# Kernel tuning notes

Hardware: AMD Instinct MI355X
Metric: run time of the kernel (lower is better)

## Reference

```python
import jax, jax.numpy as jnp
import numpy as np

NQ, DEPTH = 4, 2
C64 = jnp.complex64


def _ry(theta):
    # theta: scalar or (B,) -> (...,2,2) complex
    h = theta.astype(jnp.float32) / 2
    c, s = jnp.cos(h).astype(C64), jnp.sin(h).astype(C64)
    return jnp.stack([jnp.stack([c, -s], -1), jnp.stack([s, c], -1)], -2)


def _rot(phi, theta, omega):
    # PennyLane Rot = RZ(omega) @ RY(theta) @ RZ(phi), scalars -> (2,2) complex
    h = theta / 2
    c, s = jnp.cos(h), jnp.sin(h)
    ep = jnp.exp(-0.5j * (phi + omega).astype(C64))
    em = jnp.exp(0.5j * (phi - omega).astype(C64))
    return jnp.array(1.0, C64) * jnp.stack([
        jnp.stack([ep * c, -em * s], -1),
        jnp.stack([jnp.conj(em) * s, jnp.conj(ep) * c], -1)], -2)


def _apply_1q(state, U, wire):
    # state: (B,2,2,2,2); U: (2,2) or (B,2,2)
    s = jnp.moveaxis(state, wire + 1, -1)
    if U.ndim == 2:
        s = jnp.einsum('ij,bklmj->bklmi', U, s)
    else:
        s = jnp.einsum('bij,bklmj->bklmi', U, s)
    return jnp.moveaxis(s, -1, wire + 1)


def _cnot(state, ctrl, tgt):
    s = jnp.moveaxis(state, [ctrl + 1, tgt + 1], [-2, -1])
    s = s.at[..., 1, :].set(s[..., 1, ::-1])
    return jnp.moveaxis(s, [-2, -1], [ctrl + 1, tgt + 1])


def _circuit(x, q_weights):
    B = x.shape[0]
    state = jnp.zeros((B, 2, 2, 2, 2), C64).at[:, 0, 0, 0, 0].set(1.0)
    # angle encoding: RY(x[:, w]) on wire w (batched gates)
    for w in range(NQ):
        state = _apply_1q(state, _ry(x[:, w]), w)
    # variational layers
    for layer in range(DEPTH):
        for w in range(NQ):
            U = _rot(q_weights[layer, w, 0], q_weights[layer, w, 1], q_weights[layer, w, 2])
            state = _apply_1q(state, U, w)
        for w in range(NQ - 1):
            state = _cnot(state, w, w + 1)
        state = _cnot(state, NQ - 1, 0)  # num_qubits > 2 wrap-around
    # expval PauliZ on each wire
    probs = jnp.abs(state) ** 2  # (B,2,2,2,2) float32
    z = jnp.array([1.0, -1.0], jnp.float32)
    outs = [jnp.einsum('bijkl,' + 'ijkl'[w] + '->b', probs, z) for w in range(NQ)]
    return jnp.stack(outs, axis=1).astype(x.dtype)  # (B, 4)


def setup_inputs() -> dict:
    key = jax.random.key(0)
    k1, k2 = jax.random.split(key)
    B = 2_000_000
    x = jax.random.uniform(k1, (B, NQ), jnp.float32, minval=0.0, maxval=np.pi)
    q_weights = jax.random.normal(k2, (DEPTH, NQ, 3), jnp.float32) * 0.01
    return {"x": x, "q_weights": q_weights}


def reference(x, q_weights):
    return _circuit(x, q_weights)
```

## Files before the change

### kernel.cpp

```cpp
#include <hip/hip_runtime.h>

#define NQ 4
#define DEPTH 2
#define K 4
#define BLK 256

typedef float v2f __attribute__((ext_vector_type(2)));

__device__ __forceinline__ float2 cmul(float2 a, float2 b) {
    return make_float2(a.x * b.x - a.y * b.y, a.x * b.y + a.y * b.x);
}
__device__ __forceinline__ float2 cadd(float2 a, float2 b) {
    return make_float2(a.x + b.x, a.y + b.y);
}

__device__ __forceinline__ void build_u_col(const float* __restrict__ qw, int col,
                                            float2 amp[16]) {
#pragma unroll
    for (int i = 0; i < 16; i++)
        amp[i] = make_float2((i == col) ? 1.f : 0.f, 0.f);

#pragma unroll
    for (int layer = 0; layer < DEPTH; layer++) {
#pragma unroll
        for (int w = 0; w < NQ; w++) {
            const float* g = qw + (layer * NQ + w) * 3;
            float phi = g[0], theta = g[1], omega = g[2];
            float ch, sh, sp, cp, sm, cm;
            __sincosf(0.5f * theta, &sh, &ch);
            __sincosf(-0.5f * (phi + omega), &sp, &cp);
            __sincosf(0.5f * (phi - omega), &sm, &cm);
            float2 U00 = make_float2(cp * ch, sp * ch);
            float2 U01 = make_float2(-cm * sh, -sm * sh);
            float2 U10 = make_float2(cm * sh, -sm * sh);
            float2 U11 = make_float2(cp * ch, -sp * ch);
            const int mask = 8 >> w;
#pragma unroll
            for (int i0 = 0; i0 < 16; i0++) {
                if (i0 & mask) continue;
                const int i1 = i0 | mask;
                float2 a0 = amp[i0], a1 = amp[i1];
                amp[i0] = cadd(cmul(U00, a0), cmul(U01, a1));
                amp[i1] = cadd(cmul(U10, a0), cmul(U11, a1));
            }
        }
#pragma unroll
        for (int c = 0; c < NQ; c++) {
            const int t = (c + 1) & 3;
            const int cmsk = 8 >> c, tmsk = 8 >> t;
#pragma unroll
            for (int i = 0; i < 16; i++) {
                if ((i & cmsk) && !(i & tmsk)) {
                    float2 tmp = amp[i];
                    amp[i] = amp[i | tmsk];
                    amp[i | tmsk] = tmp;
                }
            }
        }
    }
}

__global__ void build_u_kernel(const float* __restrict__ qw, v2f* __restrict__ Ug) {
    const int tid = threadIdx.x;
    if (tid < 16) {
        float2 amp[16];
        build_u_col(qw, tid, amp);
#pragma unroll
        for (int i = 0; i < 16; i++) {
            v2f u; u.x = amp[i].x; u.y = amp[i].y;
            Ug[i * 16 + tid] = u;
        }
    }
}

__device__ __forceinline__ void vqc_main_body(const float* __restrict__ x,
                                              const v2f* Um,
                                              float* __restrict__ out, int B) {
    const int tid = threadIdx.x;
    const int base = blockIdx.x * (BLK * K) + tid;

    float psi[K][16];
    bool valid[K];
#pragma unroll
    for (int k = 0; k < K; k++) {
        const int b = base + k * BLK;
        valid[k] = (b < B);
        float4 xv = valid[k] ? ((const float4*)x)[b] : make_float4(0.f, 0.f, 0.f, 0.f);
        float c0, s0, c1, s1, c2, s2, c3, s3;
        __sincosf(0.5f * xv.x, &s0, &c0);
        __sincosf(0.5f * xv.y, &s1, &c1);
        __sincosf(0.5f * xv.z, &s2, &c2);
        __sincosf(0.5f * xv.w, &s3, &c3);
        const float a01[4] = {c0 * c1, c0 * s1, s0 * c1, s0 * s1};
        const float a23[4] = {c2 * c3, c2 * s3, s2 * c3, s2 * s3};
#pragma unroll
        for (int i = 0; i < 16; i++)
            psi[k][i] = a01[i >> 2] * a23[i & 3];
    }

    float ow[NQ][K];
#pragma unroll
    for (int w = 0; w < NQ; w++)
#pragma unroll
        for (int k = 0; k < K; k++) ow[w][k] = 0.f;

#pragma unroll 1
    for (int iq = 0; iq < 4; iq++) {
        v2f acc[4][K];
#pragma unroll
        for (int ii = 0; ii < 4; ii++)
#pragma unroll
            for (int k = 0; k < K; k++) acc[ii][k] = (v2f)0.f;

        const v2f* Urow = Um + iq * 64;
#pragma unroll
        for (int j = 0; j < 16; j++) {
#pragma unroll
            for (int ii = 0; ii < 4; ii++) {
                const v2f u = Urow[ii * 16 + j];
#pragma unroll
                for (int k = 0; k < K; k++)
                    acc[ii][k] += u * psi[k][j];
            }
        }

        const float sg0 = (iq & 2) ? -1.f : 1.f;
        const float sg1 = (iq & 1) ? -1.f : 1.f;
#pragma unroll
        for (int k = 0; k < K; k++) {
            float p0 = acc[0][k].x * acc[0][k].x + acc[0][k].y * acc[0][k].y;
            float p1 = acc[1][k].x * acc[1][k].x + acc[1][k].y * acc[1][k].y;
            float p2 = acc[2][k].x * acc[2][k].x + acc[2][k].y * acc[2][k].y;
            float p3 = acc[3][k].x * acc[3][k].x + acc[3][k].y * acc[3][k].y;
            float s01 = p0 + p1, d01 = p0 - p1;
            float s23 = p2 + p3, d23 = p2 - p3;
            float ssum = s01 + s23;
            ow[2][k] += s01 - s23;
            ow[3][k] += d01 + d23;
            ow[0][k] = fmaf(sg0, ssum, ow[0][k]);
            ow[1][k] = fmaf(sg1, ssum, ow[1][k]);
        }
    }

#pragma unroll
    for (int k = 0; k < K; k++) {
        const int b = base + k * BLK;
        if (valid[k])
            ((float4*)out)[b] = make_float4(ow[0][k], ow[1][k], ow[2][k], ow[3][k]);
    }
}

__global__ __launch_bounds__(BLK) void vqc_main(const float* __restrict__ x,
                                                const v2f* __restrict__ Ug,
                                                float* __restrict__ out, int B) {
    __shared__ v2f Um[256];
    Um[threadIdx.x] = Ug[threadIdx.x];
    __syncthreads();
    vqc_main_body(x, Um, out, B);
}

__global__ __launch_bounds__(BLK) void vqc_fused(const float* __restrict__ x,
                                                 const float* __restrict__ qw,
                                                 float* __restrict__ out, int B) {
    __shared__ v2f Um[256];
    if (threadIdx.x < 16) {
        float2 amp[16];
        build_u_col(qw, threadIdx.x, amp);
#pragma unroll
        for (int i = 0; i < 16; i++) {
            v2f u; u.x = amp[i].x; u.y = amp[i].y;
            Um[i * 16 + threadIdx.x] = u;
        }
    }
    __syncthreads();
    vqc_main_body(x, Um, out, B);
}

extern "C" void kernel_launch(void* const* d_in, const int* in_sizes, int n_in,
                              void* d_out, int out_size, void* d_ws, size_t ws_size,
                              hipStream_t stream) {
    const float* x  = (const float*)d_in[0];
    const float* qw = (const float*)d_in[1];
    float* out = (float*)d_out;
    const int B = in_sizes[0] / NQ;
    const int blocks = (B + BLK * K - 1) / (BLK * K);

    if (ws_size >= 256 * sizeof(v2f)) {
        v2f* Ug = (v2f*)d_ws;
        build_u_kernel<<<1, 64, 0, stream>>>(qw, Ug);
        vqc_main<<<blocks, BLK, 0, stream>>>(x, Ug, out, B);
    } else {
        vqc_fused<<<blocks, BLK, 0, stream>>>(x, qw, out, B);
    }
}
```

Baseline: 113.7 us.

## Pack batch pairs into packed-FP32 FMAs and recompute psi on the fly

Restructures the 16x16 complex matvec so that two batch elements share each v_pk_fma_f32. op_sel broadcasts the real or imaginary part of a U entry across the pair. Psi amplitudes are no longer stored as 16 floats per element; they are rebuilt from the separable a01*a23 factors inside the loop, which cuts register pressure. U is read as 128-bit LDS loads. Sin/cos switch to raw hardware builtins with a prescaled argument, and launch bounds now request 4 blocks per CU. The hand-written inline asm limits compiler scheduling, and the raw trig builtins may lose some accuracy.

```diff
diff --git a/kernel.cpp b/kernel.cpp
--- a/kernel.cpp
+++ b/kernel.cpp
@@ -2,10 +2,28 @@
 
 #define NQ 4
 #define DEPTH 2
+#define BLK 256
 #define K 4
-#define BLK 256
 
 typedef float v2f __attribute__((ext_vector_type(2)));
+typedef float v4f __attribute__((ext_vector_type(4)));
+
+__device__ __forceinline__ void pk_fma_lo(v2f& acc, v2f u, v2f b) {
+    asm("v_pk_fma_f32 %0, %1, %2, %0 op_sel:[0,0,0] op_sel_hi:[0,1,1]"
+        : "+v"(acc) : "v"(u), "v"(b));
+}
+__device__ __forceinline__ void pk_fma_hi(v2f& acc, v2f u, v2f b) {
+    asm("v_pk_fma_f32 %0, %1, %2, %0 op_sel:[1,0,0] op_sel_hi:[1,1,1]"
+        : "+v"(acc) : "v"(u), "v"(b));
+}
+__device__ __forceinline__ v2f pk_mul(v2f a, v2f b) {
+    v2f d;
+    asm("v_pk_mul_f32 %0, %1, %2" : "=v"(d) : "v"(a), "v"(b));
+    return d;
+}
+__device__ __forceinline__ void pk_fma(v2f& acc, v2f a, v2f b) {
+    asm("v_pk_fma_f32 %0, %1, %2, %0" : "+v"(acc) : "v"(a), "v"(b));
+}
 
 __device__ __forceinline__ float2 cmul(float2 a, float2 b) {
     return make_float2(a.x * b.x - a.y * b.y, a.x * b.y + a.y * b.x);
@@ -74,106 +92,136 @@
 }
 
 __device__ __forceinline__ void vqc_main_body(const float* __restrict__ x,
-                                              const v2f* Um,
+                                              const v4f* UmS,
                                               float* __restrict__ out, int B) {
     const int tid = threadIdx.x;
     const int base = blockIdx.x * (BLK * K) + tid;
 
-    float psi[K][16];
-    bool valid[K];
+    float4 xv[K];
+    bool val[K];
 #pragma unroll
     for (int k = 0; k < K; k++) {
         const int b = base + k * BLK;
-        valid[k] = (b < B);
-        float4 xv = valid[k] ? ((const float4*)x)[b] : make_float4(0.f, 0.f, 0.f, 0.f);
-        float c0, s0, c1, s1, c2, s2, c3, s3;
-        __sincosf(0.5f * xv.x, &s0, &c0);
-        __sincosf(0.5f * xv.y, &s1, &c1);
-        __sincosf(0.5f * xv.z, &s2, &c2);
-        __sincosf(0.5f * xv.w, &s3, &c3);
-        const float a01[4] = {c0 * c1, c0 * s1, s0 * c1, s0 * s1};
-        const float a23[4] = {c2 * c3, c2 * s3, s2 * c3, s2 * s3};
-#pragma unroll
-        for (int i = 0; i < 16; i++)
-            psi[k][i] = a01[i >> 2] * a23[i & 3];
-    }
-
-    float ow[NQ][K];
-#pragma unroll
-    for (int w = 0; w < NQ; w++)
-#pragma unroll
-        for (int k = 0; k < K; k++) ow[w][k] = 0.f;
+        val[k] = (b < B);
+        xv[k] = val[k] ? ((const float4*)x)[b] : make_float4(0.f, 0.f, 0.f, 0.f);
+    }
+
+    const float R = 0.07957747154594767f;
+    float a01[K][4], a23[K][4];
+#pragma unroll
+    for (int k = 0; k < K; k++) {
+        float s0 = __builtin_amdgcn_sinf(xv[k].x * R), c0 = __builtin_amdgcn_cosf(xv[k].x * R);
+        float s1 = __builtin_amdgcn_sinf(xv[k].y * R), c1 = __builtin_amdgcn_cosf(xv[k].y * R);
+        float s2 = __builtin_amdgcn_sinf(xv[k].z * R), c2 = __builtin_amdgcn_cosf(xv[k].z * R);
+        float s3 = __builtin_amdgcn_sinf(xv[k].w * R), c3 = __builtin_amdgcn_cosf(xv[k].w * R);
+        a01[k][0] = c0 * c1; a01[k][1] = c0 * s1; a01[k][2] = s0 * c1; a01[k][3] = s0 * s1;
+        a23[k][0] = c2 * c3; a23[k][1] = c2 * s3; a23[k][2] = s2 * c3; a23[k][3] = s2 * s3;
+    }
+    v2f a01p[2][4], a23p[2][4];
+#pragma unroll
+    for (int p = 0; p < 2; p++)
+#pragma unroll
+        for (int i = 0; i < 4; i++) {
+            v2f t0; t0.x = a01[2 * p][i]; t0.y = a01[2 * p + 1][i]; a01p[p][i] = t0;
+            v2f t1; t1.x = a23[2 * p][i]; t1.y = a23[2 * p + 1][i]; a23p[p][i] = t1;
+        }
+
+    v2f ow[4][2];
+#pragma unroll
+    for (int w = 0; w < 4; w++)
+#pragma unroll
+        for (int p = 0; p < 2; p++) ow[w][p] = (v2f)0.f;
 
 #pragma unroll 1
     for (int iq = 0; iq < 4; iq++) {
-        v2f acc[4][K];
+        const v4f* rowp = UmS + iq * 32;
+        v2f accre[4][2], accim[4][2];
 #pragma unroll
         for (int ii = 0; ii < 4; ii++)
 #pragma unroll
-            for (int k = 0; k < K; k++) acc[ii][k] = (v2f)0.f;
-
-        const v2f* Urow = Um + iq * 64;
-#pragma unroll
-        for (int j = 0; j < 16; j++) {
+            for (int p = 0; p < 2; p++) { accre[ii][p] = (v2f)0.f; accim[ii][p] = (v2f)0.f; }
+
+#pragma unroll
+        for (int jp = 0; jp < 8; jp++) {
+            const int j0 = 2 * jp, j1 = 2 * jp + 1;
+            v2f ps0[2], ps1[2];
+#pragma unroll
+            for (int p = 0; p < 2; p++) {
+                ps0[p] = pk_mul(a01p[p][j0 >> 2], a23p[p][j0 & 3]);
+                ps1[p] = pk_mul(a01p[p][j1 >> 2], a23p[p][j1 & 3]);
+            }
 #pragma unroll
             for (int ii = 0; ii < 4; ii++) {
-                const v2f u = Urow[ii * 16 + j];
-#pragma unroll
-                for (int k = 0; k < K; k++)
-                    acc[ii][k] += u * psi[k][j];
-            }
-        }
-
-        const float sg0 = (iq & 2) ? -1.f : 1.f;
-        const float sg1 = (iq & 1) ? -1.f : 1.f;
-#pragma unroll
-        for (int k = 0; k < K; k++) {
-            float p0 = acc[0][k].x * acc[0][k].x + acc[0][k].y * acc[0][k].y;
-            float p1 = acc[1][k].x * acc[1][k].x + acc[1][k].y * acc[1][k].y;
-            float p2 = acc[2][k].x * acc[2][k].x + acc[2][k].y * acc[2][k].y;
-            float p3 = acc[3][k].x * acc[3][k].x + acc[3][k].y * acc[3][k].y;
-            float s01 = p0 + p1, d01 = p0 - p1;
-            float s23 = p2 + p3, d23 = p2 - p3;
-            float ssum = s01 + s23;
-            ow[2][k] += s01 - s23;
-            ow[3][k] += d01 + d23;
-            ow[0][k] = fmaf(sg0, ssum, ow[0][k]);
-            ow[1][k] = fmaf(sg1, ssum, ow[1][k]);
-        }
-    }
-
-#pragma unroll
-    for (int k = 0; k < K; k++) {
-        const int b = base + k * BLK;
-        if (valid[k])
-            ((float4*)out)[b] = make_float4(ow[0][k], ow[1][k], ow[2][k], ow[3][k]);
-    }
-}
-
-__global__ __launch_bounds__(BLK) void vqc_main(const float* __restrict__ x,
-                                                const v2f* __restrict__ Ug,
-                                                float* __restrict__ out, int B) {
-    __shared__ v2f Um[256];
-    Um[threadIdx.x] = Ug[threadIdx.x];
+                v4f q = rowp[ii * 8 + jp];
+                v2f u0 = __builtin_shufflevector(q, q, 0, 1);
+                v2f u1 = __builtin_shufflevector(q, q, 2, 3);
+#pragma unroll
+                for (int p = 0; p < 2; p++) {
+                    pk_fma_lo(accre[ii][p], u0, ps0[p]);
+                    pk_fma_hi(accim[ii][p], u0, ps0[p]);
+                    pk_fma_lo(accre[ii][p], u1, ps1[p]);
+                    pk_fma_hi(accim[ii][p], u1, ps1[p]);
+                }
+            }
+        }
+
+#pragma unroll
+        for (int p = 0; p < 2; p++) {
+            v2f p0 = pk_mul(accre[0][p], accre[0][p]); pk_fma(p0, accim[0][p], accim[0][p]);
+            v2f p1 = pk_mul(accre[1][p], accre[1][p]); pk_fma(p1, accim[1][p], accim[1][p]);
+            v2f p2 = pk_mul(accre[2][p], accre[2][p]); pk_fma(p2, accim[2][p], accim[2][p]);
+            v2f p3 = pk_mul(accre[3][p], accre[3][p]); pk_fma(p3, accim[3][p], accim[3][p]);
+            v2f s01 = p0 + p1, d01 = p0 - p1;
+            v2f s23 = p2 + p3, d23 = p2 - p3;
+            v2f ssum = s01 + s23;
+            ow[2][p] += s01 - s23;
+            ow[3][p] += d01 + d23;
+            if (iq & 2) ow[0][p] -= ssum; else ow[0][p] += ssum;
+            if (iq & 1) ow[1][p] -= ssum; else ow[1][p] += ssum;
+        }
+    }
+
+#pragma unroll
+    for (int p = 0; p < 2; p++)
+#pragma unroll
+        for (int e = 0; e < 2; e++) {
+            const int k = 2 * p + e;
+            const int b = base + k * BLK;
+            if (val[k]) {
+                float4 o;
+                o.x = (e == 0) ? ow[0][p].x : ow[0][p].y;
+                o.y = (e == 0) ? ow[1][p].x : ow[1][p].y;
+                o.z = (e == 0) ? ow[2][p].x : ow[2][p].y;
+                o.w = (e == 0) ? ow[3][p].x : ow[3][p].y;
+                ((float4*)out)[b] = o;
+            }
+        }
+}
+
+__global__ __launch_bounds__(BLK, 4) void vqc_main(const float* __restrict__ x,
+                                                   const v4f* __restrict__ Ug,
+                                                   float* __restrict__ out, int B) {
+    __shared__ v4f UmS[128];
+    if (threadIdx.x < 128) UmS[threadIdx.x] = Ug[threadIdx.x];
     __syncthreads();
-    vqc_main_body(x, Um, out, B);
-}
-
-__global__ __launch_bounds__(BLK) void vqc_fused(const float* __restrict__ x,
-                                                 const float* __restrict__ qw,
-                                                 float* __restrict__ out, int B) {
-    __shared__ v2f Um[256];
+    vqc_main_body(x, UmS, out, B);
+}
+
+__global__ void vqc_fused(const float* __restrict__ x, const float* __restrict__ qw,
+                          float* __restrict__ out, int B) {
+    __shared__ v4f UmS[128];
     if (threadIdx.x < 16) {
         float2 amp[16];
         build_u_col(qw, threadIdx.x, amp);
+        v2f* Um2 = (v2f*)UmS;
 #pragma unroll
         for (int i = 0; i < 16; i++) {
             v2f u; u.x = amp[i].x; u.y = amp[i].y;
-            Um[i * 16 + threadIdx.x] = u;
+            Um2[i * 16 + threadIdx.x] = u;
         }
     }
     __syncthreads();
-    vqc_main_body(x, Um, out, B);
+    vqc_main_body(x, UmS, out, B);
 }
 
 extern "C" void kernel_launch(void* const* d_in, const int* in_sizes, int n_in,
@@ -188,7 +236,7 @@
     if (ws_size >= 256 * sizeof(v2f)) {
         v2f* Ug = (v2f*)d_ws;
         build_u_kernel<<<1, 64, 0, stream>>>(qw, Ug);
-        vqc_main<<<blocks, BLK, 0, stream>>>(x, Ug, out, B);
+        vqc_main<<<blocks, BLK, 0, stream>>>(x, (const v4f*)Ug, out, B);
     } else {
         vqc_fused<<<blocks, BLK, 0, stream>>>(x, qw, out, B);
     }
```

Measured after the change: 110.1 us. 3.2% less time.
